# Optimization experiments

Measured on AMD Instinct MI355X. Metric: run time of the kernel, lower is better.

Reference implementation:

```python
import jax, jax.numpy as jnp
import numpy as np

N = 512          # grid size
L = 1.0          # domain length
DX = L / (N - 1)
DT = 5e-7        # satisfies CFL: dt <= dx^2 / (4 * max_alpha)
NUM_STEPS = 500
MB = 256         # material_boundary[1]: columns [0, MB) are material 1


def setup_inputs() -> dict:
    key = jax.random.key(0)
    u0 = jax.random.normal(key, (N, N), dtype=jnp.float32)
    return {
        "u0": u0,
        "k1": jnp.ones((1,), jnp.float32) * 1.0,
        "k2": jnp.ones((1,), jnp.float32) * 1.5,
        "alpha1": jnp.ones((1,), jnp.float32) * 1.0,
        "alpha2": jnp.ones((1,), jnp.float32) * 0.8,
    }


def _step(T, alpha_col, k1, k2):
    # 5-point Laplacian on interior points
    dx2 = jnp.float32(DX * DX)
    lap = (T[:-2, 1:-1] + T[2:, 1:-1] + T[1:-1, :-2] + T[1:-1, 2:]
           - 4.0 * T[1:-1, 1:-1]) / dx2
    # explicit Euler update with per-column diffusivity alpha(j)
    Tn = T.at[1:-1, 1:-1].set(T[1:-1, 1:-1]
                              + jnp.float32(DT) * alpha_col[None, 1:-1] * lap)
    # interface continuity: column MB-1 set from flux-weighted neighbors of OLD T
    i = MB - 1
    Tn = Tn.at[:, i].set((k1 * T[:, i + 1] + k2 * T[:, i - 1]) / (k1 + k2))
    # Dirichlet zero boundaries
    Tn = Tn.at[0, :].set(0.0).at[-1, :].set(0.0)
    Tn = Tn.at[:, 0].set(0.0).at[:, -1].set(0.0)
    return Tn


def reference(u0, k1, k2, alpha1, alpha2):
    k1 = k1.reshape(())
    k2 = k2.reshape(())
    a1 = alpha1.reshape(())
    a2 = alpha2.reshape(())
    # material_map: columns [0, MB) -> alpha1, else alpha2 (rows identical)
    alpha_col = jnp.where(jnp.arange(N) < MB, a1, a2).astype(u0.dtype)

    def body(T, _):
        Tn = _step(T, alpha_col, k1, k2)
        return Tn, Tn

    # intermediate_steps[1:] == states after steps 1..num_steps-1
    _, outs = jax.lax.scan(body, u0, None, length=NUM_STEPS - 1)
    return outs  # [NUM_STEPS-1, N, N]
```

## Files before the change

kernel.cpp:

```cpp
#include <hip/hip_runtime.h>


#define GN 512
#define NSTEPS 499
#define MBND 256
#define INV_DX2 261121.0f
#define DT 5e-7f

#define TO 32
#define KMAX 16
#define LOAD 64
#define LSTR 68

__device__ __forceinline__ void lds_barrier() {
    asm volatile("s_waitcnt lgkmcnt(0)" ::: "memory");
    __builtin_amdgcn_s_barrier();
    asm volatile("" ::: "memory");
}

template<int STEPS>
__global__ __launch_bounds__(1024) void heat_multi(
    const float* __restrict__ Tin, float* __restrict__ outBase,
    const float* __restrict__ k1p, const float* __restrict__ k2p,
    const float* __restrict__ a1p, const float* __restrict__ a2p)
{
    __shared__ float buf[2][LOAD][LSTR];

    const int t  = threadIdx.x;
    const int bi = blockIdx.x >> 4;
    const int bj = blockIdx.x & 15;
    const int gi0 = bi * TO - KMAX;
    const int gj0 = bj * TO - KMAX;

    {
        const int r  = t >> 4;
        const int c4 = (t & 15) * 4;
        const bool innerB = (gi0 >= 0) && (gi0 + LOAD <= GN) &&
                            (gj0 >= 0) && (gj0 + LOAD <= GN);
        if (innerB) {
            float4 v = *(const float4*)&Tin[(size_t)(gi0 + r) * GN + (gj0 + c4)];
            *(float4*)&buf[0][r][c4] = v;
        } else {
            const int gi = gi0 + r;
            #pragma unroll
            for (int e = 0; e < 4; ++e) {
                const int gj = gj0 + c4 + e;
                buf[0][r][c4 + e] = (gi >= 0 && gi < GN && gj >= 0 && gj < GN)
                                    ? Tin[(size_t)gi * GN + gj] : 0.0f;
            }
        }
    }

    const int tx = t & 15, ty = t >> 4;
    const int lj0 = tx * 4;
    const int ra = (ty == 0) ? 0 : ty - 1;
    const int rb = (ty == LOAD - 1) ? LOAD - 1 : ty + 1;

    const float k1 = k1p[0], k2 = k2p[0];
    const float a1 = a1p[0], a2 = a2p[0];
    const float invk = 1.0f / (k1 + k2);

    float Acol[4]; bool ifc[4], bc[4];
    #pragma unroll
    for (int j = 0; j < 4; ++j) {
        const int gj = gj0 + lj0 + j;
        Acol[j] = (DT * INV_DX2) * ((gj < MBND) ? a1 : a2);
        ifc[j] = (gj == MBND - 1);
        bc[j]  = (gj <= 0) || (gj >= GN - 1);
    }
    const int gi = gi0 + ty;
    const bool brow = (gi <= 0) || (gi >= GN - 1);

    const bool anyIfc = (gj0 <= MBND - 1) && (MBND - 1 < gj0 + LOAD);
    const bool anyBC  = (gj0 <= 0) || (gj0 + LOAD >= GN);
    const bool anyBR  = (gi0 <= 0) || (gi0 + LOAD >= GN);

    const bool owned = (tx >= 4) && (tx < 12) && (ty >= KMAX) && (ty < KMAX + TO);
    float* dst = outBase + ((size_t)gi * GN + (gj0 + lj0));

    lds_barrier();
    float R[4];
    {
        const float4 v = *(const float4*)&buf[0][ty][lj0];
        R[0] = v.x; R[1] = v.y; R[2] = v.z; R[3] = v.w;
    }

    #pragma unroll
    for (int s = 1; s <= STEPS; ++s) {
        const float lf = __shfl_up(R[3], 1);
        const float rg = __shfl_down(R[0], 1);

        const float (*B)[LSTR] = buf[(s - 1) & 1];
        const float4 top = *(const float4*)&B[ra][lj0];
        const float4 bot = *(const float4*)&B[rb][lj0];

        const float le0 = lf,   le1 = R[0], le2 = R[1], le3 = R[2];
        const float ri0 = R[1], ri1 = R[2], ri2 = R[3], ri3 = rg;

        float Nv[4];
        Nv[0] = fmaf(Acol[0], fmaf(-4.0f, R[0], (top.x + bot.x) + (le0 + ri0)), R[0]);
        Nv[1] = fmaf(Acol[1], fmaf(-4.0f, R[1], (top.y + bot.y) + (le1 + ri1)), R[1]);
        Nv[2] = fmaf(Acol[2], fmaf(-4.0f, R[2], (top.z + bot.z) + (le2 + ri2)), R[2]);
        Nv[3] = fmaf(Acol[3], fmaf(-4.0f, R[3], (top.w + bot.w) + (le3 + ri3)), R[3]);

        if (anyIfc) {
            const float le[4] = {le0, le1, le2, le3};
            const float ri[4] = {ri0, ri1, ri2, ri3};
            #pragma unroll
            for (int j = 0; j < 4; ++j)
                Nv[j] = ifc[j] ? (k1 * ri[j] + k2 * le[j]) * invk : Nv[j];
        }
        if (anyBC) {
            #pragma unroll
            for (int j = 0; j < 4; ++j) Nv[j] = bc[j] ? 0.0f : Nv[j];
        }
        if (anyBR) {
            #pragma unroll
            for (int j = 0; j < 4; ++j) Nv[j] = brow ? 0.0f : Nv[j];
        }
        R[0] = Nv[0]; R[1] = Nv[1]; R[2] = Nv[2]; R[3] = Nv[3];

        float (*W)[LSTR] = buf[s & 1];
        *(float4*)&W[ty][lj0] = make_float4(R[0], R[1], R[2], R[3]);

        if (owned) *(float4*)dst = make_float4(R[0], R[1], R[2], R[3]);
        dst += (size_t)GN * GN;

        if (s < STEPS) lds_barrier();
    }
}

extern "C" void kernel_launch(void* const* d_in, const int* in_sizes, int n_in,
                              void* d_out, int out_size, void* d_ws, size_t ws_size,
                              hipStream_t stream)
{
    const float* u0 = (const float*)d_in[0];
    const float* k1 = (const float*)d_in[1];
    const float* k2 = (const float*)d_in[2];
    const float* a1 = (const float*)d_in[3];
    const float* a2 = (const float*)d_in[4];
    float* out = (float*)d_out;

    const int pts = GN * GN;
    const float* src = u0;
    int done = 0;
    while (done < NSTEPS) {
        int steps = NSTEPS - done;
        if (steps > KMAX) steps = KMAX;
        float* ob = out + (size_t)done * pts;
        if (steps == KMAX)
            heat_multi<KMAX><<<256, 1024, 0, stream>>>(src, ob, k1, k2, a1, a2);
        else
            heat_multi<3><<<256, 1024, 0, stream>>>(src, ob, k1, k2, a1, a2);
        src = ob + (size_t)(steps - 1) * pts;
        done += steps;
    }
}
```

Measured before the change: 362.8 us.

## Fuse two time steps per LDS exchange with redundant neighbor-row compute and DPP shifts

Each thread now loads rows ±1 and ±2 from shared memory and computes three rows for the first step, then its own row for the second step. This halves the number of LDS writes and barriers per time step pair. Lane-neighbor exchange uses DPP row shifts instead of __shfl. The trade is about three times the stencil arithmetic in the first substep. The DPP row_shr/shl bound_ctrl semantics at 16-lane row edges must match the 16-thread row layout.

```diff
diff --git a/kernel.cpp b/kernel.cpp
--- a/kernel.cpp
+++ b/kernel.cpp
@@ -18,13 +18,53 @@
     asm volatile("" ::: "memory");
 }
 
+__device__ __forceinline__ float dpp_row_shr1(float x) {
+    int v = __builtin_amdgcn_update_dpp(__float_as_int(x), __float_as_int(x),
+                                        0x111, 0xf, 0xf, false);
+    return __int_as_float(v);
+}
+__device__ __forceinline__ float dpp_row_shl1(float x) {
+    int v = __builtin_amdgcn_update_dpp(__float_as_int(x), __float_as_int(x),
+                                        0x101, 0xf, 0xf, false);
+    return __int_as_float(v);
+}
+
+struct Prm {
+    float Ac[4]; bool ifc[4]; bool bcl[4];
+    float k1, k2, invk;
+    bool aI, aC, aR;
+};
+
+__device__ __forceinline__ void srow(const float x[4], const float up[4],
+                                     const float dn[4], float out[4],
+                                     const Prm& p, bool brF)
+{
+    const float lf = dpp_row_shr1(x[3]);
+    const float rg = dpp_row_shl1(x[0]);
+    const float le[4] = {lf, x[0], x[1], x[2]};
+    const float ri[4] = {x[1], x[2], x[3], rg};
+    #pragma unroll
+    for (int j = 0; j < 4; ++j) {
+        float v = fmaf(p.Ac[j], fmaf(-4.0f, x[j], (up[j] + dn[j]) + (le[j] + ri[j])), x[j]);
+        if (p.aI) v = p.ifc[j] ? (p.k1 * ri[j] + p.k2 * le[j]) * p.invk : v;
+        if (p.aC) v = p.bcl[j] ? 0.0f : v;
+        if (p.aR) v = brF ? 0.0f : v;
+        out[j] = v;
+    }
+}
+
+__device__ __forceinline__ void ld4(float d[4], const float* s) {
+    const float4 v = *(const float4*)s;
+    d[0] = v.x; d[1] = v.y; d[2] = v.z; d[3] = v.w;
+}
+
 template<int STEPS>
 __global__ __launch_bounds__(1024) void heat_multi(
     const float* __restrict__ Tin, float* __restrict__ outBase,
     const float* __restrict__ k1p, const float* __restrict__ k2p,
     const float* __restrict__ a1p, const float* __restrict__ a2p)
 {
-    __shared__ float buf[2][LOAD][LSTR];
+    __shared__ float Sb[2][LOAD][LSTR];
 
     const int t  = threadIdx.x;
     const int bi = blockIdx.x >> 4;
@@ -32,101 +72,100 @@
     const int gi0 = bi * TO - KMAX;
     const int gj0 = bj * TO - KMAX;
 
+    const int tx = t & 15, ty = t >> 4;
+    const int lj0 = tx * 4;
+
+    float C[4];
     {
-        const int r  = t >> 4;
-        const int c4 = (t & 15) * 4;
         const bool innerB = (gi0 >= 0) && (gi0 + LOAD <= GN) &&
                             (gj0 >= 0) && (gj0 + LOAD <= GN);
+        float4 v;
         if (innerB) {
-            float4 v = *(const float4*)&Tin[(size_t)(gi0 + r) * GN + (gj0 + c4)];
-            *(float4*)&buf[0][r][c4] = v;
+            v = *(const float4*)&Tin[(size_t)(gi0 + ty) * GN + (gj0 + lj0)];
         } else {
-            const int gi = gi0 + r;
+            const int gi_ = gi0 + ty;
+            float tmp[4];
             #pragma unroll
             for (int e = 0; e < 4; ++e) {
-                const int gj = gj0 + c4 + e;
-                buf[0][r][c4 + e] = (gi >= 0 && gi < GN && gj >= 0 && gj < GN)
-                                    ? Tin[(size_t)gi * GN + gj] : 0.0f;
+                const int gj_ = gj0 + lj0 + e;
+                tmp[e] = ((unsigned)gi_ < GN && (unsigned)gj_ < GN)
+                         ? Tin[(size_t)gi_ * GN + gj_] : 0.0f;
             }
+            v = make_float4(tmp[0], tmp[1], tmp[2], tmp[3]);
+        }
+        *(float4*)&Sb[0][ty][lj0] = v;
+        C[0] = v.x; C[1] = v.y; C[2] = v.z; C[3] = v.w;
+    }
+
+    const int rm1 = (ty >= 1) ? ty - 1 : 0;
+    const int rm2 = (ty >= 2) ? ty - 2 : 0;
+    const int rp1 = (ty <= LOAD - 2) ? ty + 1 : LOAD - 1;
+    const int rp2 = (ty <= LOAD - 3) ? ty + 2 : LOAD - 1;
+
+    Prm p;
+    p.k1 = k1p[0]; p.k2 = k2p[0];
+    const float a1 = a1p[0], a2 = a2p[0];
+    p.invk = 1.0f / (p.k1 + p.k2);
+    #pragma unroll
+    for (int j = 0; j < 4; ++j) {
+        const int gj_ = gj0 + lj0 + j;
+        p.Ac[j]  = (DT * INV_DX2) * ((gj_ < MBND) ? a1 : a2);
+        p.ifc[j] = (gj_ == MBND - 1);
+        p.bcl[j] = (gj_ <= 0) || (gj_ >= GN - 1);
+    }
+    p.aI = (bj == 7) || (bj == 8);
+    p.aC = (bj == 0) || (bj == 15);
+    p.aR = (bi == 0) || (bi == 15);
+
+    const int gi = gi0 + ty;
+    const bool brM = (gi - 1 <= 0) || (gi - 1 >= GN - 1);
+    const bool br0 = (gi     <= 0) || (gi     >= GN - 1);
+    const bool brP = (gi + 1 <= 0) || (gi + 1 >= GN - 1);
+
+    const bool own = (tx >= 4) && (tx < 12) && (ty >= KMAX) && (ty < KMAX + TO);
+    float* dst = outBase + ((long)gi * GN + (gj0 + lj0));
+
+    lds_barrier();
+
+    constexpr int NG = STEPS / 2;
+    #pragma unroll
+    for (int g = 0; g < NG; ++g) {
+        const float (*Rb)[LSTR] = Sb[g & 1];
+        float (*Wb)[LSTR] = Sb[(g + 1) & 1];
+
+        float A[4], B[4], D[4], E[4];
+        ld4(A, &Rb[rm2][lj0]);
+        ld4(B, &Rb[rm1][lj0]);
+        ld4(D, &Rb[rp1][lj0]);
+        ld4(E, &Rb[rp2][lj0]);
+
+        float nB[4], nC[4], nD[4];
+        srow(B, A, C, nB, p, brM);
+        srow(C, B, D, nC, p, br0);
+        srow(D, C, E, nD, p, brP);
+        if (own) *(float4*)dst = make_float4(nC[0], nC[1], nC[2], nC[3]);
+        dst += (long)GN * GN;
+
+        float n2[4];
+        srow(nC, nB, nD, n2, p, br0);
+        if (own) *(float4*)dst = make_float4(n2[0], n2[1], n2[2], n2[3]);
+        dst += (long)GN * GN;
+
+        C[0] = n2[0]; C[1] = n2[1]; C[2] = n2[2]; C[3] = n2[3];
+
+        if (g < NG - 1 || STEPS == 3) {
+            *(float4*)&Wb[ty][lj0] = make_float4(C[0], C[1], C[2], C[3]);
+            lds_barrier();
         }
     }
 
-    const int tx = t & 15, ty = t >> 4;
-    const int lj0 = tx * 4;
-    const int ra = (ty == 0) ? 0 : ty - 1;
-    const int rb = (ty == LOAD - 1) ? LOAD - 1 : ty + 1;
-
-    const float k1 = k1p[0], k2 = k2p[0];
-    const float a1 = a1p[0], a2 = a2p[0];
-    const float invk = 1.0f / (k1 + k2);
-
-    float Acol[4]; bool ifc[4], bc[4];
-    #pragma unroll
-    for (int j = 0; j < 4; ++j) {
-        const int gj = gj0 + lj0 + j;
-        Acol[j] = (DT * INV_DX2) * ((gj < MBND) ? a1 : a2);
-        ifc[j] = (gj == MBND - 1);
-        bc[j]  = (gj <= 0) || (gj >= GN - 1);
-    }
-    const int gi = gi0 + ty;
-    const bool brow = (gi <= 0) || (gi >= GN - 1);
-
-    const bool anyIfc = (gj0 <= MBND - 1) && (MBND - 1 < gj0 + LOAD);
-    const bool anyBC  = (gj0 <= 0) || (gj0 + LOAD >= GN);
-    const bool anyBR  = (gi0 <= 0) || (gi0 + LOAD >= GN);
-
-    const bool owned = (tx >= 4) && (tx < 12) && (ty >= KMAX) && (ty < KMAX + TO);
-    float* dst = outBase + ((size_t)gi * GN + (gj0 + lj0));
-
-    lds_barrier();
-    float R[4];
-    {
-        const float4 v = *(const float4*)&buf[0][ty][lj0];
-        R[0] = v.x; R[1] = v.y; R[2] = v.z; R[3] = v.w;
-    }
-
-    #pragma unroll
-    for (int s = 1; s <= STEPS; ++s) {
-        const float lf = __shfl_up(R[3], 1);
-        const float rg = __shfl_down(R[0], 1);
-
-        const float (*B)[LSTR] = buf[(s - 1) & 1];
-        const float4 top = *(const float4*)&B[ra][lj0];
-        const float4 bot = *(const float4*)&B[rb][lj0];
-
-        const float le0 = lf,   le1 = R[0], le2 = R[1], le3 = R[2];
-        const float ri0 = R[1], ri1 = R[2], ri2 = R[3], ri3 = rg;
-
-        float Nv[4];
-        Nv[0] = fmaf(Acol[0], fmaf(-4.0f, R[0], (top.x + bot.x) + (le0 + ri0)), R[0]);
-        Nv[1] = fmaf(Acol[1], fmaf(-4.0f, R[1], (top.y + bot.y) + (le1 + ri1)), R[1]);
-        Nv[2] = fmaf(Acol[2], fmaf(-4.0f, R[2], (top.z + bot.z) + (le2 + ri2)), R[2]);
-        Nv[3] = fmaf(Acol[3], fmaf(-4.0f, R[3], (top.w + bot.w) + (le3 + ri3)), R[3]);
-
-        if (anyIfc) {
-            const float le[4] = {le0, le1, le2, le3};
-            const float ri[4] = {ri0, ri1, ri2, ri3};
-            #pragma unroll
-            for (int j = 0; j < 4; ++j)
-                Nv[j] = ifc[j] ? (k1 * ri[j] + k2 * le[j]) * invk : Nv[j];
-        }
-        if (anyBC) {
-            #pragma unroll
-            for (int j = 0; j < 4; ++j) Nv[j] = bc[j] ? 0.0f : Nv[j];
-        }
-        if (anyBR) {
-            #pragma unroll
-            for (int j = 0; j < 4; ++j) Nv[j] = brow ? 0.0f : Nv[j];
-        }
-        R[0] = Nv[0]; R[1] = Nv[1]; R[2] = Nv[2]; R[3] = Nv[3];
-
-        float (*W)[LSTR] = buf[s & 1];
-        *(float4*)&W[ty][lj0] = make_float4(R[0], R[1], R[2], R[3]);
-
-        if (owned) *(float4*)dst = make_float4(R[0], R[1], R[2], R[3]);
-        dst += (size_t)GN * GN;
-
-        if (s < STEPS) lds_barrier();
+    if constexpr (STEPS == 3) {
+        float B[4], D[4];
+        ld4(B, &Sb[1][rm1][lj0]);
+        ld4(D, &Sb[1][rp1][lj0]);
+        float nC[4];
+        srow(C, B, D, nC, p, br0);
+        if (own) *(float4*)dst = make_float4(nC[0], nC[1], nC[2], nC[3]);
     }
 }
 
```

Result: slower. 387.3 us (+6.7%).
